# Kernel optimization log

Hardware: AMD Instinct MI355X
Metric: run time of the kernel (lower is better)

## Reference

```python
import jax, jax.numpy as jnp
import numpy as np

B, D, M, W, R, NW = 64, 512, 1024, 64, 4, 1
EPS = 1e-6


def setup_inputs() -> dict:
    key = jax.random.key(0)
    ks = jax.random.split(key, 26)
    outs = {'wv': NW * W, 'ev': NW * W, 'fg': R, 'ag': NW, 'wg': NW,
            'rm': R * (1 + 2 * NW), 'ws': NW, 'rs': R, 'wk': NW * W, 'rk': R * W}
    d = {}
    for i, (name, o) in enumerate(outs.items()):
        d[name + '_w'] = jax.random.normal(ks[2 * i], (D, o), jnp.float32) / np.sqrt(D)
        d[name + '_b'] = jax.random.normal(ks[2 * i + 1], (o,), jnp.float32) * 0.1
    d['x'] = jax.random.normal(ks[20], (B, D), jnp.float32)
    d['prev_memory'] = jax.random.normal(ks[21], (B, M, W), jnp.float32)
    d['prev_read_weights'] = jax.nn.softmax(jax.random.normal(ks[22], (B, R, M), jnp.float32), -1)
    d['prev_write_weights'] = jax.nn.softmax(jax.random.normal(ks[23], (B, NW, M), jnp.float32), -1)
    d['prev_link'] = jnp.zeros((B, NW, M, M), jnp.float32)
    d['prev_precedence'] = jnp.zeros((B, NW, M), jnp.float32)
    d['prev_usage'] = jax.random.uniform(ks[24], (B, M), jnp.float32)
    return d


def _cosine_weights(memory, keys, strengths):
    # memory [b,M,W], keys [b,H,W], strengths [b,H] (softplus already applied)
    dot = jnp.einsum('bhw,bmw->bhm', keys, memory)
    mn = jnp.sqrt(jnp.sum(memory * memory, -1) + EPS)   # [b,M]
    kn = jnp.sqrt(jnp.sum(keys * keys, -1) + EPS)       # [b,H]
    sim = dot / (kn[:, :, None] * mn[:, None, :])
    return jax.nn.softmax(sim * strengths[..., None], axis=-1)


def _allocation(usage):
    # usage [b,M] -> allocation weights [b,M] (DNC Freeness)
    usage = EPS + (1.0 - EPS) * usage
    idx = jnp.argsort(usage, axis=-1)                       # ascending usage
    sorted_usage = jnp.take_along_axis(usage, idx, -1)
    excl_cumprod = jnp.concatenate(
        [jnp.ones_like(sorted_usage[:, :1]),
         jnp.cumprod(sorted_usage, axis=-1)[:, :-1]], axis=-1)
    sorted_alloc = (1.0 - sorted_usage) * excl_cumprod
    inv = jnp.argsort(idx, axis=-1)                         # invert permutation
    return jnp.take_along_axis(sorted_alloc, inv, -1)


def _write_allocation_weights(usage, write_gates):
    # write_gates [b,NW]; sequential allocation across (few) write heads
    allocs = []
    for i in range(NW):
        a = _allocation(usage)
        allocs.append(a)
        usage = usage + (1.0 - usage) * write_gates[:, i:i + 1] * a
    return jnp.stack(allocs, axis=1)  # [b,NW,M]


def _forward(x, prev_memory, prev_read_weights, prev_write_weights, prev_link,
             prev_precedence, prev_usage, wv_w, wv_b, ev_w, ev_b, fg_w, fg_b,
             ag_w, ag_b, wg_w, wg_b, rm_w, rm_b, ws_w, ws_b, rs_w, rs_b,
             wk_w, wk_b, rk_w, rk_b):
    b = x.shape[0]
    lin = lambda w, bb: x @ w + bb
    write_vectors = lin(wv_w, wv_b).reshape(b, NW, W)
    erase_vectors = jax.nn.sigmoid(lin(ev_w, ev_b)).reshape(b, NW, W)
    free_gate = jax.nn.sigmoid(lin(fg_w, fg_b))            # [b,R]
    allocation_gate = jax.nn.sigmoid(lin(ag_w, ag_b))      # [b,NW]
    write_gate = jax.nn.sigmoid(lin(wg_w, wg_b))           # [b,NW]
    read_mode = jax.nn.softmax(lin(rm_w, rm_b).reshape(b, R, 1 + 2 * NW), -1)
    write_keys = lin(wk_w, wk_b).reshape(b, NW, W)
    write_strengths = jax.nn.softplus(lin(ws_w, ws_b))     # [b,NW]
    read_keys = lin(rk_w, rk_b).reshape(b, R, W)
    read_strengths = jax.nn.softplus(lin(rs_w, rs_b))      # [b,R]

    # --- Freeness usage update ---
    write_agg = 1.0 - jnp.prod(1.0 - prev_write_weights, axis=1)   # [b,M]
    usage_after_write = prev_usage + (1.0 - prev_usage) * write_agg
    phi = jnp.prod(1.0 - free_gate[..., None] * prev_read_weights, axis=1)
    usage = usage_after_write * phi

    # --- write weights ---
    wcw = _cosine_weights(prev_memory, write_keys, write_strengths)  # [b,NW,M]
    waw = _write_allocation_weights(usage, allocation_gate * write_gate)
    ag = allocation_gate[..., None]
    wg = write_gate[..., None]
    write_weights = wg * (ag * waw + (1.0 - ag) * wcw)               # [b,NW,M]

    # --- erase and write ---
    weighted_resets = write_weights[..., None] * erase_vectors[:, :, None, :]
    reset_gate = jnp.prod(1.0 - weighted_resets, axis=1)             # [b,M,W]
    memory = prev_memory * reset_gate + jnp.einsum(
        'bwm,bwd->bmd', write_weights, write_vectors)

    # --- temporal linkage ---
    ww_sum = jnp.sum(write_weights, -1, keepdims=True)               # [b,NW,1]
    precedence = (1.0 - ww_sum) * prev_precedence + write_weights
    w_i = write_weights[..., None]          # [b,NW,M,1]
    w_j = write_weights[:, :, None, :]      # [b,NW,1,M]
    p_j = prev_precedence[:, :, None, :]    # [b,NW,1,M]
    link = (1.0 - w_i - w_j) * prev_link + w_i * p_j
    link = link * (1.0 - jnp.eye(M, dtype=link.dtype))

    # --- read weights ---
    rcw = _cosine_weights(memory, read_keys, read_strengths)         # [b,R,M]
    fwd = jnp.einsum('brj,bwij->brwi', prev_read_weights, link)
    bwd = jnp.einsum('brj,bwji->brwi', prev_read_weights, link)
    backward_mode = read_mode[:, :, :NW]
    forward_mode = read_mode[:, :, NW:2 * NW]
    content_mode = read_mode[:, :, 2 * NW]
    read_weights = (content_mode[..., None] * rcw
                    + jnp.sum(forward_mode[..., None] * fwd, axis=2)
                    + jnp.sum(backward_mode[..., None] * bwd, axis=2))
    read_words = jnp.einsum('brm,bmd->brd', read_weights, memory)
    return read_words, memory, read_weights, write_weights, link, precedence, usage


def reference(x, prev_memory, prev_read_weights, prev_write_weights, prev_link,
              prev_precedence, prev_usage, wv_w, wv_b, ev_w, ev_b, fg_w, fg_b,
              ag_w, ag_b, wg_w, wg_b, rm_w, rm_b, ws_w, ws_b, rs_w, rs_b,
              wk_w, wk_b, rk_w, rk_b):
    return _forward(x, prev_memory, prev_read_weights, prev_write_weights,
                    prev_link, prev_precedence, prev_usage, wv_w, wv_b, ev_w,
                    ev_b, fg_w, fg_b, ag_w, ag_b, wg_w, wg_b, rm_w, rm_b,
                    ws_w, ws_b, rs_w, rs_b, wk_w, wk_b, rk_w, rk_b)
```

## Files before the change

kernel.cpp:

```cpp
#include <hip/hip_runtime.h>

#define NB 64
#define ND 512
#define NM 1024
#define NR 4
#define EPSF 1e-6f

static const size_t O_WV    = 0;
static const size_t O_EV    = 4096;
static const size_t O_FG    = 8192;
static const size_t O_AG    = 8448;
static const size_t O_WG    = 8512;
static const size_t O_RM    = 9344;
static const size_t O_WK    = 10112;
static const size_t O_WSTR  = 14208;
static const size_t O_RK    = 14272;
static const size_t O_RSTR  = 30656;
static const size_t O_WAW   = 96448;
static const size_t O_WWGT  = 161984;
static const size_t O_PREC  = 227520;
static const size_t O_MN    = 293056;
static const size_t O_FWD   = 358592;
static const size_t O_BWD   = 620736;
static const size_t O_RWTS  = 882880;
static const size_t O_BWDP  = 1145024;

static const size_t OO_RWORDS = 0;
static const size_t OO_MEM    = 16384;
static const size_t OO_RW     = 4210688;
static const size_t OO_WWGT   = 4472832;
static const size_t OO_LINK   = 4538368;
static const size_t OO_PREC   = 71647232;
static const size_t OO_USAGE  = 71712768;

__device__ __forceinline__ float sigm(float x) { return 1.f / (1.f + expf(-x)); }
__device__ __forceinline__ float softplus_(float x) { return fmaxf(x, 0.f) + log1pf(expf(-fabsf(x))); }

__global__ void k_controller(
    const float* __restrict__ x,
    const float* __restrict__ wv_w, const float* __restrict__ wv_b,
    const float* __restrict__ ev_w, const float* __restrict__ ev_b,
    const float* __restrict__ fg_w, const float* __restrict__ fg_b,
    const float* __restrict__ ag_w, const float* __restrict__ ag_b,
    const float* __restrict__ wg_w, const float* __restrict__ wg_b,
    const float* __restrict__ rm_w, const float* __restrict__ rm_b,
    const float* __restrict__ ws_w, const float* __restrict__ ws_b,
    const float* __restrict__ rs_w, const float* __restrict__ rs_b,
    const float* __restrict__ wk_w, const float* __restrict__ wk_b,
    const float* __restrict__ rk_w, const float* __restrict__ rk_b,
    float* __restrict__ wsb)
{
    int b = blockIdx.x;
    int c = threadIdx.x;
    __shared__ float rmraw[12];
    if (c < 471) {
        const float* wp; const float* bp; int O; int cl; int act; size_t dsto = 0;
        if (c < 64)       { wp = wv_w; bp = wv_b; O = 64;  cl = c;       act = 0; dsto = O_WV + b * 64 + cl; }
        else if (c < 128) { wp = ev_w; bp = ev_b; O = 64;  cl = c - 64;  act = 1; dsto = O_EV + b * 64 + cl; }
        else if (c < 132) { wp = fg_w; bp = fg_b; O = 4;   cl = c - 128; act = 1; dsto = O_FG + b * 4 + cl; }
        else if (c < 133) { wp = ag_w; bp = ag_b; O = 1;   cl = 0;       act = 1; dsto = O_AG + b; }
        else if (c < 134) { wp = wg_w; bp = wg_b; O = 1;   cl = 0;       act = 1; dsto = O_WG + b; }
        else if (c < 146) { wp = rm_w; bp = rm_b; O = 12;  cl = c - 134; act = 3; }
        else if (c < 147) { wp = ws_w; bp = ws_b; O = 1;   cl = 0;       act = 2; dsto = O_WSTR + b; }
        else if (c < 151) { wp = rs_w; bp = rs_b; O = 4;   cl = c - 147; act = 2; dsto = O_RSTR + b * 4 + cl; }
        else if (c < 215) { wp = wk_w; bp = wk_b; O = 64;  cl = c - 151; act = 0; dsto = O_WK + b * 64 + cl; }
        else              { wp = rk_w; bp = rk_b; O = 256; cl = c - 215; act = 0; dsto = O_RK + b * 256 + cl; }
        float acc = bp[cl];
        const float* xb = x + b * ND;
        for (int d = 0; d < ND; ++d) acc += xb[d] * wp[d * O + cl];
        if (act == 1) acc = sigm(acc);
        else if (act == 2) acc = softplus_(acc);
        if (act == 3) rmraw[cl] = acc;
        else wsb[dsto] = acc;
    }
    __syncthreads();
    if (c < 4) {
        float a0 = rmraw[c * 3 + 0], a1 = rmraw[c * 3 + 1], a2 = rmraw[c * 3 + 2];
        float mx = fmaxf(a0, fmaxf(a1, a2));
        float e0 = expf(a0 - mx), e1 = expf(a1 - mx), e2 = expf(a2 - mx);
        float s = e0 + e1 + e2;
        float* dst = wsb + O_RM + b * 12 + c * 3;
        dst[0] = e0 / s; dst[1] = e1 / s; dst[2] = e2 / s;
    }
}

__global__ __launch_bounds__(1024) void k_alloc(
    const float* __restrict__ pu, const float* __restrict__ prw,
    const float* __restrict__ pww, float* __restrict__ wsb, float* __restrict__ out)
{
    __shared__ float sv[1024];
    __shared__ int   si[1024];
    __shared__ float sp[1024];
    int b = blockIdx.x, t = threadIdx.x;
    int idx = b * NM + t;
    float u0 = pu[idx];
    float uaw = u0 + (1.f - u0) * pww[idx];
    float phi = 1.f;
#pragma unroll
    for (int r = 0; r < NR; r++)
        phi *= (1.f - wsb[O_FG + b * 4 + r] * prw[(b * 4 + r) * NM + t]);
    float u = uaw * phi;
    out[OO_USAGE + idx] = u;
    sv[t] = EPSF + (1.0f - EPSF) * u;
    si[t] = t;
    __syncthreads();
    for (int k = 2; k <= 1024; k <<= 1) {
        for (int j = k >> 1; j > 0; j >>= 1) {
            int ixj = t ^ j;
            if (ixj > t) {
                float a = sv[t], c = sv[ixj];
                int ia = si[t], ic = si[ixj];
                bool asc = (t & k) == 0;
                bool gt = (a > c) || (a == c && ia > ic);
                if (gt == asc) { sv[t] = c; sv[ixj] = a; si[t] = ic; si[ixj] = ia; }
            }
            __syncthreads();
        }
    }
    sp[t] = sv[t];
    __syncthreads();
    for (int off = 1; off < 1024; off <<= 1) {
        float v = sp[t];
        float o = (t >= off) ? sp[t - off] : 1.f;
        __syncthreads();
        sp[t] = v * o;
        __syncthreads();
    }
    float excl = (t == 0) ? 1.f : sp[t - 1];
    wsb[O_WAW + b * NM + si[t]] = (1.f - sv[t]) * excl;
}

__global__ __launch_bounds__(256) void k_writew(
    const float* __restrict__ pm, const float* __restrict__ pp,
    float* __restrict__ wsb, float* __restrict__ out)
{
    int b = blockIdx.x, t = threadIdx.x;
    __shared__ float red[256];
    const float* wk = wsb + O_WK + b * 64;
    float kn2 = 0.f;
#pragma unroll
    for (int w = 0; w < 64; w++) { float v = wk[w]; kn2 += v * v; }
    float kn = sqrtf(kn2 + EPSF);
    float wstr = wsb[O_WSTR + b];
    float sim[4];
#pragma unroll
    for (int k = 0; k < 4; k++) {
        int m = t + k * 256;
        const float* row = pm + ((size_t)(b * NM + m)) * 64;
        float dot = 0.f, mn2 = 0.f;
        for (int w = 0; w < 64; w++) { float pv = row[w]; dot += wk[w] * pv; mn2 += pv * pv; }
        sim[k] = dot / (kn * sqrtf(mn2 + EPSF)) * wstr;
    }
    float lm = fmaxf(fmaxf(sim[0], sim[1]), fmaxf(sim[2], sim[3]));
    red[t] = lm; __syncthreads();
    for (int s = 128; s > 0; s >>= 1) { if (t < s) red[t] = fmaxf(red[t], red[t + s]); __syncthreads(); }
    float mx = red[0]; __syncthreads();
    float e[4]; float ls = 0.f;
#pragma unroll
    for (int k = 0; k < 4; k++) { e[k] = expf(sim[k] - mx); ls += e[k]; }
    red[t] = ls; __syncthreads();
    for (int s = 128; s > 0; s >>= 1) { if (t < s) red[t] += red[t + s]; __syncthreads(); }
    float inv = 1.f / red[0]; __syncthreads();
    float ag = wsb[O_AG + b], wg = wsb[O_WG + b];
    float wwv[4]; float lsum = 0.f;
#pragma unroll
    for (int k = 0; k < 4; k++) {
        int m = t + k * 256;
        float wcw = e[k] * inv;
        float waw = wsb[O_WAW + b * NM + m];
        float w_ = wg * (ag * waw + (1.f - ag) * wcw);
        wwv[k] = w_; lsum += w_;
        wsb[O_WWGT + b * NM + m] = w_;
        out[OO_WWGT + b * NM + m] = w_;
    }
    red[t] = lsum; __syncthreads();
    for (int s = 128; s > 0; s >>= 1) { if (t < s) red[t] += red[t + s]; __syncthreads(); }
    float wwsum = red[0];
#pragma unroll
    for (int k = 0; k < 4; k++) {
        int m = t + k * 256;
        float pr = (1.f - wwsum) * pp[b * NM + m] + wwv[k];
        wsb[O_PREC + b * NM + m] = pr;
        out[OO_PREC + b * NM + m] = pr;
    }
}

__global__ void k_mem(const float* __restrict__ pm, float* __restrict__ wsb, float* __restrict__ out)
{
    int gid = blockIdx.x * 256 + threadIdx.x;
    int b = gid >> 10;
    float w_ = wsb[O_WWGT + gid];
    const float* evp = wsb + O_EV + b * 64;
    const float* wvp = wsb + O_WV + b * 64;
    const float* pmr = pm + (size_t)gid * 64;
    float* outr = out + OO_MEM + (size_t)gid * 64;
    float s = 0.f;
    for (int w = 0; w < 64; w++) {
        float val = pmr[w] * (1.f - w_ * evp[w]) + w_ * wvp[w];
        outr[w] = val;
        s += val * val;
    }
    wsb[O_MN + gid] = sqrtf(s + EPSF);
}

__global__ __launch_bounds__(256) void k_linkfb(
    const float* __restrict__ pl, const float* __restrict__ pp,
    const float* __restrict__ prw, float* __restrict__ wsb, float* __restrict__ out)
{
    int b = blockIdx.x, rg = blockIdx.y;
    int t = threadIdx.x, wave = t >> 6, lane = t & 63;
    const float* wwb = wsb + O_WWGT + b * NM;
    const float* ppb = pp + b * NM;
    const float* rwb = prw + (size_t)b * 4 * NM;
    float4 wj[4], pj[4], rwc[4][4];
#pragma unroll
    for (int s = 0; s < 4; s++) {
        int c4 = s * 256 + lane * 4;
        wj[s] = *(const float4*)(wwb + c4);
        pj[s] = *(const float4*)(ppb + c4);
#pragma unroll
        for (int h = 0; h < 4; h++)
            rwc[h][s] = *(const float4*)(rwb + h * NM + c4);
    }
    float4 bacc[4][4];
#pragma unroll
    for (int h = 0; h < 4; h++)
#pragma unroll
        for (int s = 0; s < 4; s++) bacc[h][s] = make_float4(0.f, 0.f, 0.f, 0.f);

    int rowbase = rg * 64 + wave * 16;
    float4 vin[4];
    {
        const float* pr0 = pl + ((size_t)(b * NM + rowbase)) * NM;
#pragma unroll
        for (int s = 0; s < 4; s++) vin[s] = *(const float4*)(pr0 + s * 256 + lane * 4);
    }
    for (int rr = 0; rr < 16; rr++) {
        int row = rowbase + rr;
        float4 vc[4];
#pragma unroll
        for (int s = 0; s < 4; s++) vc[s] = vin[s];
        if (rr < 15) {
            const float* pn = pl + ((size_t)(b * NM + row + 1)) * NM;
#pragma unroll
            for (int s = 0; s < 4; s++) vin[s] = *(const float4*)(pn + s * 256 + lane * 4);
        }
        float wi = wwb[row];
        float rh0 = rwb[0 * NM + row], rh1 = rwb[1 * NM + row];
        float rh2 = rwb[2 * NM + row], rh3 = rwb[3 * NM + row];
        float a = 1.f - wi;
        float* lkrow = out + OO_LINK + ((size_t)(b * NM + row)) * NM;
        float f0 = 0.f, f1 = 0.f, f2 = 0.f, f3 = 0.f;
#pragma unroll
        for (int s = 0; s < 4; s++) {
            int c4 = s * 256 + lane * 4;
            float4 lv;
            lv.x = (a - wj[s].x) * vc[s].x + wi * pj[s].x; if (row == c4)     lv.x = 0.f;
            lv.y = (a - wj[s].y) * vc[s].y + wi * pj[s].y; if (row == c4 + 1) lv.y = 0.f;
            lv.z = (a - wj[s].z) * vc[s].z + wi * pj[s].z; if (row == c4 + 2) lv.z = 0.f;
            lv.w = (a - wj[s].w) * vc[s].w + wi * pj[s].w; if (row == c4 + 3) lv.w = 0.f;
            *(float4*)(lkrow + c4) = lv;
            f0 += rwc[0][s].x * lv.x + rwc[0][s].y * lv.y + rwc[0][s].z * lv.z + rwc[0][s].w * lv.w;
            f1 += rwc[1][s].x * lv.x + rwc[1][s].y * lv.y + rwc[1][s].z * lv.z + rwc[1][s].w * lv.w;
            f2 += rwc[2][s].x * lv.x + rwc[2][s].y * lv.y + rwc[2][s].z * lv.z + rwc[2][s].w * lv.w;
            f3 += rwc[3][s].x * lv.x + rwc[3][s].y * lv.y + rwc[3][s].z * lv.z + rwc[3][s].w * lv.w;
            bacc[0][s].x += rh0 * lv.x; bacc[0][s].y += rh0 * lv.y; bacc[0][s].z += rh0 * lv.z; bacc[0][s].w += rh0 * lv.w;
            bacc[1][s].x += rh1 * lv.x; bacc[1][s].y += rh1 * lv.y; bacc[1][s].z += rh1 * lv.z; bacc[1][s].w += rh1 * lv.w;
            bacc[2][s].x += rh2 * lv.x; bacc[2][s].y += rh2 * lv.y; bacc[2][s].z += rh2 * lv.z; bacc[2][s].w += rh2 * lv.w;
            bacc[3][s].x += rh3 * lv.x; bacc[3][s].y += rh3 * lv.y; bacc[3][s].z += rh3 * lv.z; bacc[3][s].w += rh3 * lv.w;
        }
#pragma unroll
        for (int off = 32; off > 0; off >>= 1) {
            f0 += __shfl_down(f0, off); f1 += __shfl_down(f1, off);
            f2 += __shfl_down(f2, off); f3 += __shfl_down(f3, off);
        }
        if (lane == 0) {
            float4 fv = make_float4(f0, f1, f2, f3);
            *(float4*)(wsb + O_FWD + (size_t)(b * NM + row) * 4) = fv;
        }
    }
    __shared__ float redb[4][1024];
#pragma unroll
    for (int h = 0; h < 4; h++) {
        __syncthreads();
#pragma unroll
        for (int s = 0; s < 4; s++)
            *(float4*)(&redb[wave][s * 256 + lane * 4]) = bacc[h][s];
        __syncthreads();
        for (int i = t; i < 1024; i += 256) {
            float sum = redb[0][i] + redb[1][i] + redb[2][i] + redb[3][i];
            wsb[O_BWDP + ((size_t)((b * 16 + rg) * 4 + h)) * NM + i] = sum;
        }
    }
}

__global__ void k_bred(float* __restrict__ wsb)
{
    int idx = blockIdx.x * 256 + threadIdx.x;
    int b = idx >> 10, col = idx & 1023;
    float s0 = 0.f, s1 = 0.f, s2 = 0.f, s3 = 0.f;
#pragma unroll
    for (int rg = 0; rg < 16; rg++) {
        size_t base = O_BWDP + ((size_t)((b * 16 + rg) * 4)) * NM + col;
        s0 += wsb[base + 0 * NM];
        s1 += wsb[base + 1 * NM];
        s2 += wsb[base + 2 * NM];
        s3 += wsb[base + 3 * NM];
    }
    *(float4*)(wsb + O_BWD + (size_t)idx * 4) = make_float4(s0, s1, s2, s3);
}

__global__ __launch_bounds__(256) void k_readw(
    float* __restrict__ wsb, float* __restrict__ out)
{
    int b = blockIdx.x >> 2, r = blockIdx.x & 3, t = threadIdx.x;
    __shared__ float red[256];
    const float* rk = wsb + O_RK + (b * 4 + r) * 64;
    float kn2 = 0.f;
#pragma unroll
    for (int w = 0; w < 64; w++) { float v = rk[w]; kn2 += v * v; }
    float kn = sqrtf(kn2 + EPSF);
    float rstr = wsb[O_RSTR + b * 4 + r];
    float sim[4];
#pragma unroll
    for (int k = 0; k < 4; k++) {
        int m = t + k * 256;
        const float* row = out + OO_MEM + ((size_t)(b * NM + m)) * 64;
        float dot = 0.f;
        for (int w = 0; w < 64; w++) dot += rk[w] * row[w];
        sim[k] = dot / (kn * wsb[O_MN + b * NM + m]) * rstr;
    }
    float lm = fmaxf(fmaxf(sim[0], sim[1]), fmaxf(sim[2], sim[3]));
    red[t] = lm; __syncthreads();
    for (int s = 128; s > 0; s >>= 1) { if (t < s) red[t] = fmaxf(red[t], red[t + s]); __syncthreads(); }
    float mx = red[0]; __syncthreads();
    float e[4]; float ls = 0.f;
#pragma unroll
    for (int k = 0; k < 4; k++) { e[k] = expf(sim[k] - mx); ls += e[k]; }
    red[t] = ls; __syncthreads();
    for (int s = 128; s > 0; s >>= 1) { if (t < s) red[t] += red[t + s]; __syncthreads(); }
    float inv = 1.f / red[0];
    float bm = wsb[O_RM + b * 12 + r * 3 + 0];
    float fm = wsb[O_RM + b * 12 + r * 3 + 1];
    float cm = wsb[O_RM + b * 12 + r * 3 + 2];
#pragma unroll
    for (int k = 0; k < 4; k++) {
        int m = t + k * 256;
        float p = e[k] * inv;
        size_t idx4 = (size_t)(b * NM + m) * 4 + r;
        float v = cm * p + fm * wsb[O_FWD + idx4] + bm * wsb[O_BWD + idx4];
        size_t o = (size_t)(b * 4 + r) * NM + m;
        wsb[O_RWTS + o] = v;
        out[OO_RW + o] = v;
    }
}

__global__ __launch_bounds__(256) void k_rwords(
    const float* __restrict__ wsb, float* __restrict__ out)
{
    int br = blockIdx.x; int b = br >> 2;
    int t = threadIdx.x, w = t & 63, chunk = t >> 6;
    const float* rwt = wsb + O_RWTS + (size_t)br * NM;
    const float* mem = out + OO_MEM + (size_t)b * NM * 64;
    float acc = 0.f;
    int m0 = chunk * 256;
    for (int m = m0; m < m0 + 256; m++)
        acc += rwt[m] * mem[(size_t)m * 64 + w];
    __shared__ float red[4][64];
    red[chunk][w] = acc;
    __syncthreads();
    if (t < 64)
        out[OO_RWORDS + br * 64 + t] = red[0][t] + red[1][t] + red[2][t] + red[3][t];
}

extern "C" void kernel_launch(void* const* d_in, const int* in_sizes, int n_in,
                              void* d_out, int out_size, void* d_ws, size_t ws_size,
                              hipStream_t stream) {
    const float* wv_w = (const float*)d_in[0];  const float* wv_b = (const float*)d_in[1];
    const float* ev_w = (const float*)d_in[2];  const float* ev_b = (const float*)d_in[3];
    const float* fg_w = (const float*)d_in[4];  const float* fg_b = (const float*)d_in[5];
    const float* ag_w = (const float*)d_in[6];  const float* ag_b = (const float*)d_in[7];
    const float* wg_w = (const float*)d_in[8];  const float* wg_b = (const float*)d_in[9];
    const float* rm_w = (const float*)d_in[10]; const float* rm_b = (const float*)d_in[11];
    const float* ws_w = (const float*)d_in[12]; const float* ws_b = (const float*)d_in[13];
    const float* rs_w = (const float*)d_in[14]; const float* rs_b = (const float*)d_in[15];
    const float* wk_w = (const float*)d_in[16]; const float* wk_b = (const float*)d_in[17];
    const float* rk_w = (const float*)d_in[18]; const float* rk_b = (const float*)d_in[19];
    const float* x   = (const float*)d_in[20];
    const float* pm  = (const float*)d_in[21];
    const float* prw = (const float*)d_in[22];
    const float* pww = (const float*)d_in[23];
    const float* pl  = (const float*)d_in[24];
    const float* pp  = (const float*)d_in[25];
    const float* pu  = (const float*)d_in[26];
    float* out = (float*)d_out;
    float* wsb = (float*)d_ws;

    k_controller<<<NB, 512, 0, stream>>>(x, wv_w, wv_b, ev_w, ev_b, fg_w, fg_b, ag_w, ag_b,
                                         wg_w, wg_b, rm_w, rm_b, ws_w, ws_b, rs_w, rs_b,
                                         wk_w, wk_b, rk_w, rk_b, wsb);
    k_alloc<<<NB, 1024, 0, stream>>>(pu, prw, pww, wsb, out);
    k_writew<<<NB, 256, 0, stream>>>(pm, pp, wsb, out);
    k_mem<<<(NB * NM) / 256, 256, 0, stream>>>(pm, wsb, out);
    k_linkfb<<<dim3(NB, 16), 256, 0, stream>>>(pl, pp, prw, wsb, out);
    k_bred<<<(NB * NM) / 256, 256, 0, stream>>>(wsb);
    k_readw<<<NB * NR, 256, 0, stream>>>(wsb, out);
    k_rwords<<<NB * NR, 256, 0, stream>>>(wsb, out);
}
```

Before: 240.7 us.

## Fuse memory update, backward reduction and read-word kernels; use nontemporal link traffic

The memory-update kernel is folded into the write-weight kernel. The backward-partial reduction and the read-words product are folded into the read-weight kernel, which now keeps read weights in shared memory instead of going through workspace. The large link-matrix stream in k_linkfb now uses nontemporal vector loads and stores to avoid polluting the cache. This removes three launches and some workspace round-trips. The memory update now runs on only 64 blocks instead of 256, which may limit bandwidth for that 32 MB phase.

```diff
diff --git a/kernel.cpp b/kernel.cpp
--- a/kernel.cpp
+++ b/kernel.cpp
@@ -5,6 +5,8 @@
 #define NM 1024
 #define NR 4
 #define EPSF 1e-6f
+
+typedef float f4_t __attribute__((ext_vector_type(4)));
 
 static const size_t O_WV    = 0;
 static const size_t O_EV    = 4096;
@@ -21,8 +23,6 @@
 static const size_t O_PREC  = 227520;
 static const size_t O_MN    = 293056;
 static const size_t O_FWD   = 358592;
-static const size_t O_BWD   = 620736;
-static const size_t O_RWTS  = 882880;
 static const size_t O_BWDP  = 1145024;
 
 static const size_t OO_RWORDS = 0;
@@ -183,24 +183,22 @@
         wsb[O_PREC + b * NM + m] = pr;
         out[OO_PREC + b * NM + m] = pr;
     }
-}
-
-__global__ void k_mem(const float* __restrict__ pm, float* __restrict__ wsb, float* __restrict__ out)
-{
-    int gid = blockIdx.x * 256 + threadIdx.x;
-    int b = gid >> 10;
-    float w_ = wsb[O_WWGT + gid];
     const float* evp = wsb + O_EV + b * 64;
     const float* wvp = wsb + O_WV + b * 64;
-    const float* pmr = pm + (size_t)gid * 64;
-    float* outr = out + OO_MEM + (size_t)gid * 64;
-    float s = 0.f;
-    for (int w = 0; w < 64; w++) {
-        float val = pmr[w] * (1.f - w_ * evp[w]) + w_ * wvp[w];
-        outr[w] = val;
-        s += val * val;
-    }
-    wsb[O_MN + gid] = sqrtf(s + EPSF);
+#pragma unroll
+    for (int k = 0; k < 4; k++) {
+        int m = t + k * 256;
+        float w_ = wwv[k];
+        const float* pmr = pm + ((size_t)(b * NM + m)) * 64;
+        float* outr = out + OO_MEM + ((size_t)(b * NM + m)) * 64;
+        float s2 = 0.f;
+        for (int w = 0; w < 64; w++) {
+            float val = pmr[w] * (1.f - w_ * evp[w]) + w_ * wvp[w];
+            outr[w] = val;
+            s2 += val * val;
+        }
+        wsb[O_MN + b * NM + m] = sqrtf(s2 + EPSF);
+    }
 }
 
 __global__ __launch_bounds__(256) void k_linkfb(
@@ -212,38 +210,40 @@
     const float* wwb = wsb + O_WWGT + b * NM;
     const float* ppb = pp + b * NM;
     const float* rwb = prw + (size_t)b * 4 * NM;
-    float4 wj[4], pj[4], rwc[4][4];
+    f4_t wj[4], pj[4], rwc[4][4];
 #pragma unroll
     for (int s = 0; s < 4; s++) {
         int c4 = s * 256 + lane * 4;
-        wj[s] = *(const float4*)(wwb + c4);
-        pj[s] = *(const float4*)(ppb + c4);
+        wj[s] = *(const f4_t*)(wwb + c4);
+        pj[s] = *(const f4_t*)(ppb + c4);
 #pragma unroll
         for (int h = 0; h < 4; h++)
-            rwc[h][s] = *(const float4*)(rwb + h * NM + c4);
-    }
-    float4 bacc[4][4];
+            rwc[h][s] = *(const f4_t*)(rwb + h * NM + c4);
+    }
+    f4_t bacc[4][4];
 #pragma unroll
     for (int h = 0; h < 4; h++)
 #pragma unroll
-        for (int s = 0; s < 4; s++) bacc[h][s] = make_float4(0.f, 0.f, 0.f, 0.f);
+        for (int s = 0; s < 4; s++) bacc[h][s] = (f4_t){0.f, 0.f, 0.f, 0.f};
 
     int rowbase = rg * 64 + wave * 16;
-    float4 vin[4];
+    f4_t vin[4];
     {
         const float* pr0 = pl + ((size_t)(b * NM + rowbase)) * NM;
 #pragma unroll
-        for (int s = 0; s < 4; s++) vin[s] = *(const float4*)(pr0 + s * 256 + lane * 4);
+        for (int s = 0; s < 4; s++)
+            vin[s] = __builtin_nontemporal_load((const f4_t*)(pr0 + s * 256 + lane * 4));
     }
     for (int rr = 0; rr < 16; rr++) {
         int row = rowbase + rr;
-        float4 vc[4];
+        f4_t vc[4];
 #pragma unroll
         for (int s = 0; s < 4; s++) vc[s] = vin[s];
         if (rr < 15) {
             const float* pn = pl + ((size_t)(b * NM + row + 1)) * NM;
 #pragma unroll
-            for (int s = 0; s < 4; s++) vin[s] = *(const float4*)(pn + s * 256 + lane * 4);
+            for (int s = 0; s < 4; s++)
+                vin[s] = __builtin_nontemporal_load((const f4_t*)(pn + s * 256 + lane * 4));
         }
         float wi = wwb[row];
         float rh0 = rwb[0 * NM + row], rh1 = rwb[1 * NM + row];
@@ -254,12 +254,12 @@
 #pragma unroll
         for (int s = 0; s < 4; s++) {
             int c4 = s * 256 + lane * 4;
-            float4 lv;
+            f4_t lv;
             lv.x = (a - wj[s].x) * vc[s].x + wi * pj[s].x; if (row == c4)     lv.x = 0.f;
             lv.y = (a - wj[s].y) * vc[s].y + wi * pj[s].y; if (row == c4 + 1) lv.y = 0.f;
             lv.z = (a - wj[s].z) * vc[s].z + wi * pj[s].z; if (row == c4 + 2) lv.z = 0.f;
             lv.w = (a - wj[s].w) * vc[s].w + wi * pj[s].w; if (row == c4 + 3) lv.w = 0.f;
-            *(float4*)(lkrow + c4) = lv;
+            __builtin_nontemporal_store(lv, (f4_t*)(lkrow + c4));
             f0 += rwc[0][s].x * lv.x + rwc[0][s].y * lv.y + rwc[0][s].z * lv.z + rwc[0][s].w * lv.w;
             f1 += rwc[1][s].x * lv.x + rwc[1][s].y * lv.y + rwc[1][s].z * lv.z + rwc[1][s].w * lv.w;
             f2 += rwc[2][s].x * lv.x + rwc[2][s].y * lv.y + rwc[2][s].z * lv.z + rwc[2][s].w * lv.w;
@@ -275,8 +275,8 @@
             f2 += __shfl_down(f2, off); f3 += __shfl_down(f3, off);
         }
         if (lane == 0) {
-            float4 fv = make_float4(f0, f1, f2, f3);
-            *(float4*)(wsb + O_FWD + (size_t)(b * NM + row) * 4) = fv;
+            f4_t fv = (f4_t){f0, f1, f2, f3};
+            *(f4_t*)(wsb + O_FWD + (size_t)(b * NM + row) * 4) = fv;
         }
     }
     __shared__ float redb[4][1024];
@@ -285,7 +285,7 @@
         __syncthreads();
 #pragma unroll
         for (int s = 0; s < 4; s++)
-            *(float4*)(&redb[wave][s * 256 + lane * 4]) = bacc[h][s];
+            *(f4_t*)(&redb[wave][s * 256 + lane * 4]) = bacc[h][s];
         __syncthreads();
         for (int i = t; i < 1024; i += 256) {
             float sum = redb[0][i] + redb[1][i] + redb[2][i] + redb[3][i];
@@ -294,27 +294,14 @@
     }
 }
 
-__global__ void k_bred(float* __restrict__ wsb)
-{
-    int idx = blockIdx.x * 256 + threadIdx.x;
-    int b = idx >> 10, col = idx & 1023;
-    float s0 = 0.f, s1 = 0.f, s2 = 0.f, s3 = 0.f;
-#pragma unroll
-    for (int rg = 0; rg < 16; rg++) {
-        size_t base = O_BWDP + ((size_t)((b * 16 + rg) * 4)) * NM + col;
-        s0 += wsb[base + 0 * NM];
-        s1 += wsb[base + 1 * NM];
-        s2 += wsb[base + 2 * NM];
-        s3 += wsb[base + 3 * NM];
-    }
-    *(float4*)(wsb + O_BWD + (size_t)idx * 4) = make_float4(s0, s1, s2, s3);
-}
-
 __global__ __launch_bounds__(256) void k_readw(
     float* __restrict__ wsb, float* __restrict__ out)
 {
-    int b = blockIdx.x >> 2, r = blockIdx.x & 3, t = threadIdx.x;
+    int br = blockIdx.x;
+    int b = br >> 2, r = br & 3, t = threadIdx.x;
     __shared__ float red[256];
+    __shared__ float vv[1024];
+    __shared__ float red2[4][64];
     const float* rk = wsb + O_RK + (b * 4 + r) * 64;
     float kn2 = 0.f;
 #pragma unroll
@@ -347,30 +334,26 @@
     for (int k = 0; k < 4; k++) {
         int m = t + k * 256;
         float p = e[k] * inv;
-        size_t idx4 = (size_t)(b * NM + m) * 4 + r;
-        float v = cm * p + fm * wsb[O_FWD + idx4] + bm * wsb[O_BWD + idx4];
-        size_t o = (size_t)(b * 4 + r) * NM + m;
-        wsb[O_RWTS + o] = v;
-        out[OO_RW + o] = v;
-    }
-}
-
-__global__ __launch_bounds__(256) void k_rwords(
-    const float* __restrict__ wsb, float* __restrict__ out)
-{
-    int br = blockIdx.x; int b = br >> 2;
-    int t = threadIdx.x, w = t & 63, chunk = t >> 6;
-    const float* rwt = wsb + O_RWTS + (size_t)br * NM;
+        float bw = 0.f;
+#pragma unroll
+        for (int rg = 0; rg < 16; rg++)
+            bw += wsb[O_BWDP + ((size_t)((b * 16 + rg) * 4 + r)) * NM + m];
+        float fw = wsb[O_FWD + (size_t)(b * NM + m) * 4 + r];
+        float v = cm * p + fm * fw + bm * bw;
+        vv[m] = v;
+        out[OO_RW + (size_t)(b * 4 + r) * NM + m] = v;
+    }
+    __syncthreads();
+    int w = t & 63, chunk = t >> 6;
     const float* mem = out + OO_MEM + (size_t)b * NM * 64;
     float acc = 0.f;
     int m0 = chunk * 256;
     for (int m = m0; m < m0 + 256; m++)
-        acc += rwt[m] * mem[(size_t)m * 64 + w];
-    __shared__ float red[4][64];
-    red[chunk][w] = acc;
+        acc += vv[m] * mem[(size_t)m * 64 + w];
+    red2[chunk][w] = acc;
     __syncthreads();
     if (t < 64)
-        out[OO_RWORDS + br * 64 + t] = red[0][t] + red[1][t] + red[2][t] + red[3][t];
+        out[OO_RWORDS + br * 64 + t] = red2[0][t] + red2[1][t] + red2[2][t] + red2[3][t];
 }
 
 extern "C" void kernel_launch(void* const* d_in, const int* in_sizes, int n_in,
@@ -401,9 +384,6 @@
                                          wk_w, wk_b, rk_w, rk_b, wsb);
     k_alloc<<<NB, 1024, 0, stream>>>(pu, prw, pww, wsb, out);
     k_writew<<<NB, 256, 0, stream>>>(pm, pp, wsb, out);
-    k_mem<<<(NB * NM) / 256, 256, 0, stream>>>(pm, wsb, out);
     k_linkfb<<<dim3(NB, 16), 256, 0, stream>>>(pl, pp, prw, wsb, out);
-    k_bred<<<(NB * NM) / 256, 256, 0, stream>>>(wsb);
     k_readw<<<NB * NR, 256, 0, stream>>>(wsb, out);
-    k_rwords<<<NB * NR, 256, 0, stream>>>(wsb, out);
-}
+}
```

Result: faster. 224.8 us (-6.6%).
